# Kernel optimization log

Measured on AMD Instinct MI355X. Metric: run time of the kernel, lower is better.

Reference implementation:

```python
import jax, jax.numpy as jnp
import numpy as np

B, D, K = 4096, 1024, 32

def setup_inputs() -> dict:
    key = jax.random.key(0)
    k1, k2, k3, k4 = jax.random.split(key, 4)
    e1 = jax.random.normal(k1, (B, D), dtype=jnp.float32)
    e2 = jax.random.normal(k2, (B, D), dtype=jnp.float32)
    W = jax.random.normal(k3, (K, D, D), dtype=jnp.float32)
    V = jax.random.normal(k4, (2 * D, K), dtype=jnp.float32)
    b = jnp.zeros((D,), dtype=jnp.float32)
    return {"e1": e1, "e2": e2, "W": W, "V": V, "b": b}

def reference(e1, e2, W, V, b):
    batch = e1.shape[0]
    k = W.shape[0]
    # Per-slice bilinear form: btp[i, n] = sum_d e2[n,d] * (e1[n] @ W[i])[d] + sum(b)
    # (b is added elementwise before the axis-1 sum in the original, i.e. +sum(b))
    btp = jnp.einsum('bd,kde,be->kb', e1, W, e2) + jnp.sum(b)  # (k, B)
    # Original concatenates k (B,)-vectors along axis 0 then reshapes to (B, k);
    # reproduce that exact (interleaving) layout.
    btp = btp.reshape(batch, k)
    ff = jnp.concatenate([e1, e2], axis=-1) @ V  # (B, k)
    return jnp.tanh(btp + ff)
```

## Files before the change

kernel.cpp:

```cpp
#include <hip/hip_runtime.h>

#define B_SZ 4096
#define D_SZ 1024
#define K_SZ 32
#define NT   16

typedef _Float16 h16x8 __attribute__((ext_vector_type(8)));
typedef float f32x16 __attribute__((ext_vector_type(16)));
typedef float f32x4 __attribute__((ext_vector_type(4)));
typedef float f32x2 __attribute__((ext_vector_type(2)));
typedef unsigned int u32x2 __attribute__((ext_vector_type(2)));
typedef unsigned int u32x4 __attribute__((ext_vector_type(4)));
typedef unsigned short u16x4 __attribute__((ext_vector_type(4)));

#define GLOAD16(gp, sp) __builtin_amdgcn_global_load_lds( \
    (const __attribute__((address_space(1))) void*)(gp),  \
    (__attribute__((address_space(3))) void*)(sp), 16, 0, 0)

__device__ __forceinline__ void split1(float x, _Float16& h, _Float16& l) {
    h = (_Float16)x;
    l = (_Float16)((x - (float)h) * 2048.0f);
}

__global__ __launch_bounds__(256)
void ntl_prep_w(const float* __restrict__ W,
                _Float16* __restrict__ Wh, _Float16* __restrict__ Wl) {
    __shared__ float tile[64 * 69];
    const int bid = blockIdx.x;
    const int k  = bid >> 8;
    const int d0 = ((bid >> 4) & 15) << 6;
    const int e0 = (bid & 15) << 6;
    const int t  = threadIdx.x;
    const int r  = t >> 4;
    const int c4 = (t & 15) << 2;

    const float* src = W + ((size_t)k * D_SZ + d0) * D_SZ + e0;
    #pragma unroll
    for (int p = 0; p < 4; ++p) {
        f32x4 v = *(const f32x4*)(src + (size_t)(p * 16 + r) * D_SZ + c4);
        float* dst = &tile[(p * 16 + r) * 69 + c4];
        dst[0] = v[0]; dst[1] = v[1]; dst[2] = v[2]; dst[3] = v[3];
    }
    __syncthreads();
    #pragma unroll
    for (int p = 0; p < 4; ++p) {
        const int e = p * 16 + r;
        u16x4 hh, ll;
        #pragma unroll
        for (int q = 0; q < 4; ++q) {
            float v = tile[(c4 + q) * 69 + e];
            _Float16 h, l;
            split1(v, h, l);
            hh[q] = __builtin_bit_cast(unsigned short, h);
            ll[q] = __builtin_bit_cast(unsigned short, l);
        }
        const size_t o = ((size_t)k * D_SZ + e0 + e) * D_SZ + d0 + c4;
        *(u16x4*)(Wh + o) = hh;
        *(u16x4*)(Wl + o) = ll;
    }
}

__global__ __launch_bounds__(256)
void ntl_prep_e(const float* __restrict__ e1,
                _Float16* __restrict__ eh, _Float16* __restrict__ el) {
    const size_t i = ((size_t)blockIdx.x * 256 + threadIdx.x) * 4;
    f32x4 v = *(const f32x4*)(e1 + i);
    u16x4 hh, ll;
    #pragma unroll
    for (int q = 0; q < 4; ++q) {
        _Float16 h, l;
        split1(v[q], h, l);
        hh[q] = __builtin_bit_cast(unsigned short, h);
        ll[q] = __builtin_bit_cast(unsigned short, l);
    }
    *(u16x4*)(eh + i) = hh;
    *(u16x4*)(el + i) = ll;
}

__global__ __launch_bounds__(512, 2)
void ntl_bilinear4(const _Float16* __restrict__ eh, const _Float16* __restrict__ el,
                   const _Float16* __restrict__ Wh, const _Float16* __restrict__ Wl,
                   const float* __restrict__ e2, float* __restrict__ out) {
    __shared__ __align__(16) char lds[131072];

    const int bid   = blockIdx.x;
    const int xcd   = bid & 7;
    const int idx   = bid >> 3;
    const int e_t   = idx & 7;
    const int b_sub = (idx >> 3) & 1;
    const int k     = idx >> 4;
    const int b0    = (xcd * 2 + b_sub) * 256;
    const int e0    = e_t * 128;

    const int t    = threadIdx.x;
    const int l    = t & 63;
    const int w    = t >> 6;
    const int wrow = (w >> 1) * 64;
    const int wcol = (w & 1) * 64;
    const int l31  = l & 31;
    const int h5   = l >> 5;
    const int srow = l >> 3;
    const int sl   = l & 7;

    f32x16 acc1[2][2];
    f32x16 acc2[2][2];
    #pragma unroll
    for (int m = 0; m < 2; ++m)
        #pragma unroll
        for (int n = 0; n < 2; ++n) {
            #pragma unroll
            for (int j = 0; j < 16; ++j) { acc1[m][n][j] = 0.f; acc2[m][n][j] = 0.f; }
        }

    const size_t arow = (size_t)(b0 + w * 32 + srow) * D_SZ + sl * 8;
    const _Float16* gAh = eh + arow;
    const _Float16* gAl = el + arow;
    const int awOff = (w * 32 + srow) * 128 + ((sl ^ srow) << 4);

    const int gslot = sl ^ srow;
    const _Float16* gB = (w < 4 ? Wh : Wl) +
        ((size_t)k * D_SZ + e0 + (w & 3) * 32 + srow) * D_SZ + gslot * 8;
    const int bOff = (w >= 4 ? 16384 : 0) + (w & 3) * 4096;

    u32x4 arH[4], arL[4];

    {
        char* bset = lds + 65536;
        #pragma unroll
        for (int i = 0; i < 4; ++i)
            GLOAD16(gB + (size_t)i * 8 * D_SZ, bset + bOff + i * 1024);
        #pragma unroll
        for (int i = 0; i < 4; ++i) {
            arH[i] = *(const u32x4*)(gAh + (size_t)i * 8 * D_SZ);
            arL[i] = *(const u32x4*)(gAl + (size_t)i * 8 * D_SZ);
        }
    }

    for (int kt = 0; kt < NT; ++kt) {
        if (kt) {
            __builtin_amdgcn_s_barrier();
            __builtin_amdgcn_sched_barrier(0);
        }
        asm volatile("s_waitcnt vmcnt(0)" ::: "memory");
        __builtin_amdgcn_sched_barrier(0);

        #pragma unroll
        for (int i = 0; i < 4; ++i) {
            *(u32x4*)(lds + awOff + i * 1024)         = arH[i];
            *(u32x4*)(lds + 32768 + awOff + i * 1024) = arL[i];
        }

        if (kt + 1 < NT) {
            const size_t dn = (size_t)(kt + 1) * 64;
            char* bset = lds + 65536 + (((kt + 1) & 1) << 15);
            #pragma unroll
            for (int i = 0; i < 4; ++i)
                GLOAD16(gB + (size_t)i * 8 * D_SZ + dn, bset + bOff + i * 1024);
            #pragma unroll
            for (int i = 0; i < 4; ++i) {
                arH[i] = *(const u32x4*)(gAh + (size_t)i * 8 * D_SZ + dn);
                arL[i] = *(const u32x4*)(gAl + (size_t)i * 8 * D_SZ + dn);
            }
        }

        asm volatile("s_waitcnt lgkmcnt(0)" ::: "memory");
        __builtin_amdgcn_sched_barrier(0);
        __builtin_amdgcn_s_barrier();
        __builtin_amdgcn_sched_barrier(0);

        const char* Bh_ = lds + 65536 + ((kt & 1) << 15);
        const char* Bl_ = Bh_ + 16384;

        #pragma unroll
        for (int ks = 0; ks < 4; ++ks) {
            h16x8 ah[2], al[2], bh[2], bl[2];
            #pragma unroll
            for (int m = 0; m < 2; ++m) {
                const int r = wrow + m * 32 + l31;
                const int off = r * 128 + (((ks * 2 + h5) ^ (r & 7)) << 4);
                ah[m] = *(const h16x8*)(lds + off);
                al[m] = *(const h16x8*)(lds + 32768 + off);
            }
            #pragma unroll
            for (int n = 0; n < 2; ++n) {
                const int r = wcol + n * 32 + l31;
                const int off = r * 128 + (((ks * 2 + h5) ^ (r & 7)) << 4);
                bh[n] = *(const h16x8*)(Bh_ + off);
                bl[n] = *(const h16x8*)(Bl_ + off);
            }
            #pragma unroll
            for (int m = 0; m < 2; ++m)
                #pragma unroll
                for (int n = 0; n < 2; ++n) {
                    acc1[m][n] = __builtin_amdgcn_mfma_f32_32x32x16_f16(ah[m], bh[n], acc1[m][n], 0, 0, 0);
                    acc2[m][n] = __builtin_amdgcn_mfma_f32_32x32x16_f16(ah[m], bl[n], acc2[m][n], 0, 0, 0);
                    acc2[m][n] = __builtin_amdgcn_mfma_f32_32x32x16_f16(al[m], bh[n], acc2[m][n], 0, 0, 0);
                }
        }
    }

    float rsum[2][16];
    #pragma unroll
    for (int m = 0; m < 2; ++m)
        #pragma unroll
        for (int rg = 0; rg < 16; ++rg) rsum[m][rg] = 0.f;

    #pragma unroll
    for (int m = 0; m < 2; ++m) {
        #pragma unroll
        for (int n = 0; n < 2; ++n) {
            #pragma unroll
            for (int rg = 0; rg < 16; ++rg) {
                const int rowl = wrow + m * 32 + (rg & 3) + 8 * (rg >> 2) + 4 * h5;
                const int col  = e0 + wcol + n * 32 + l31;
                float tv = acc1[m][n][rg] + acc2[m][n][rg] * (1.0f / 2048.0f);
                rsum[m][rg] += tv * e2[(size_t)(b0 + rowl) * D_SZ + col];
            }
        }
    }

    #pragma unroll
    for (int m = 0; m < 2; ++m) {
        #pragma unroll
        for (int rg = 0; rg < 16; ++rg) {
            float v = rsum[m][rg];
            v += __shfl_xor(v, 1, 32);
            v += __shfl_xor(v, 2, 32);
            v += __shfl_xor(v, 4, 32);
            v += __shfl_xor(v, 8, 32);
            v += __shfl_xor(v, 16, 32);
            if (l31 == 0) {
                const int rowl = wrow + m * 32 + (rg & 3) + 8 * (rg >> 2) + 4 * h5;
                atomicAdd(out + (size_t)k * B_SZ + b0 + rowl, v);
            }
        }
    }
}

__device__ __forceinline__ int swz_fb(int row, int byte_in_row) {
    int slot = byte_in_row >> 4;
    int in   = byte_in_row & 15;
    return row * 128 + (((slot ^ (row & 7)) << 4) | in);
}
__device__ __forceinline__ void split_fb(float x, unsigned short& h, unsigned short& l) {
    _Float16 hf = (_Float16)x;
    float hff = (float)hf;
    _Float16 lf = (_Float16)((x - hff) * 2048.0f);
    h = __builtin_bit_cast(unsigned short, hf);
    l = __builtin_bit_cast(unsigned short, lf);
}
__global__ __launch_bounds__(256, 2)
void ntl_bilinear_fb(const float* __restrict__ e1, const float* __restrict__ e2,
                     const float* __restrict__ W, float* __restrict__ out) {
    __shared__ __align__(16) char smem[65536];
    char* const Ah = smem;
    char* const Al = smem + 16384;
    char* const Bh = smem + 32768;
    char* const Bl = smem + 49152;
    const int bid = blockIdx.x;
    const int k   = bid >> 8;
    const int rem = bid & 255;
    const int b0  = (rem >> 3) * 128;
    const int e0  = (rem & 7) * 128;
    const int t  = threadIdx.x;
    const int l  = t & 63;
    const int w  = t >> 6;
    const int wr = (w >> 1) * 64;
    const int wc = (w & 1) * 64;
    const int lrow = l & 15;
    const int lq   = l >> 4;
    f32x4 acc1[4][4], acc2[4][4];
    #pragma unroll
    for (int m = 0; m < 4; ++m)
        #pragma unroll
        for (int n = 0; n < 4; ++n) {
            acc1[m][n] = f32x4{0.f, 0.f, 0.f, 0.f};
            acc2[m][n] = f32x4{0.f, 0.f, 0.f, 0.f};
        }
    const int sa_row = t >> 4;
    const int sa_cg  = (t & 15) * 4;
    const int sb_e   = t & 127;
    const int sb_dg  = t >> 7;
    const float* const e1b = e1 + (size_t)b0 * D_SZ;
    const float* const wb  = W + ((size_t)k * D_SZ) * D_SZ + e0 + sb_e;
    for (int kt = 0; kt < NT; ++kt) {
        const int d0 = kt * 64;
        #pragma unroll
        for (int p = 0; p < 8; ++p) {
            const int r = sa_row + p * 16;
            f32x4 v = *(const f32x4*)(e1b + (size_t)r * D_SZ + d0 + sa_cg);
            unsigned short hh[4], ll[4];
            #pragma unroll
            for (int qq = 0; qq < 4; ++qq) split_fb(v[qq], hh[qq], ll[qq]);
            u32x2 hv = { (unsigned)hh[0] | ((unsigned)hh[1] << 16),
                         (unsigned)hh[2] | ((unsigned)hh[3] << 16) };
            u32x2 lv = { (unsigned)ll[0] | ((unsigned)ll[1] << 16),
                         (unsigned)ll[2] | ((unsigned)ll[3] << 16) };
            const int ad = swz_fb(r, sa_cg * 2);
            *(u32x2*)(Ah + ad) = hv;
            *(u32x2*)(Al + ad) = lv;
        }
        {
            const float* ws2 = wb + (size_t)(d0 + sb_dg * 32) * D_SZ;
            #pragma unroll
            for (int gg = 0; gg < 4; ++gg) {
                unsigned short hh[8], ll[8];
                #pragma unroll
                for (int i = 0; i < 8; ++i)
                    split_fb(ws2[(size_t)(gg * 8 + i) * D_SZ], hh[i], ll[i]);
                u32x4 hv = { (unsigned)hh[0] | ((unsigned)hh[1] << 16),
                             (unsigned)hh[2] | ((unsigned)hh[3] << 16),
                             (unsigned)hh[4] | ((unsigned)hh[5] << 16),
                             (unsigned)hh[6] | ((unsigned)hh[7] << 16) };
                u32x4 lv = { (unsigned)ll[0] | ((unsigned)ll[1] << 16),
                             (unsigned)ll[2] | ((unsigned)ll[3] << 16),
                             (unsigned)ll[4] | ((unsigned)ll[5] << 16),
                             (unsigned)ll[6] | ((unsigned)ll[7] << 16) };
                const int ad = swz_fb(sb_e, (sb_dg * 32 + gg * 8) * 2);
                *(u32x4*)(Bh + ad) = hv;
                *(u32x4*)(Bl + ad) = lv;
            }
        }
        __syncthreads();
        #pragma unroll
        for (int kk = 0; kk < 2; ++kk) {
            const int kb = kk * 64 + lq * 16;
            h16x8 a_h[4], a_l[4];
            #pragma unroll
            for (int m = 0; m < 4; ++m) {
                const int ad = swz_fb(wr + m * 16 + lrow, kb);
                a_h[m] = *(const h16x8*)(Ah + ad);
                a_l[m] = *(const h16x8*)(Al + ad);
            }
            #pragma unroll
            for (int n = 0; n < 4; ++n) {
                const int bd = swz_fb(wc + n * 16 + lrow, kb);
                h16x8 b_h = *(const h16x8*)(Bh + bd);
                h16x8 b_l = *(const h16x8*)(Bl + bd);
                #pragma unroll
                for (int m = 0; m < 4; ++m) {
                    acc1[m][n] = __builtin_amdgcn_mfma_f32_16x16x32_f16(a_h[m], b_h, acc1[m][n], 0, 0, 0);
                    acc2[m][n] = __builtin_amdgcn_mfma_f32_16x16x32_f16(a_h[m], b_l, acc2[m][n], 0, 0, 0);
                    acc2[m][n] = __builtin_amdgcn_mfma_f32_16x16x32_f16(a_l[m], b_h, acc2[m][n], 0, 0, 0);
                }
            }
        }
        __syncthreads();
    }
    float rsum[16];
    #pragma unroll
    for (int i = 0; i < 16; ++i) rsum[i] = 0.f;
    #pragma unroll
    for (int m = 0; m < 4; ++m) {
        #pragma unroll
        for (int n = 0; n < 4; ++n) {
            const int col = e0 + wc + n * 16 + lrow;
            #pragma unroll
            for (int j = 0; j < 4; ++j) {
                const int row = b0 + wr + m * 16 + lq * 4 + j;
                float tv = acc1[m][n][j] + acc2[m][n][j] * (1.0f / 2048.0f);
                rsum[m * 4 + j] += tv * e2[(size_t)row * D_SZ + col];
            }
        }
    }
    #pragma unroll
    for (int i = 0; i < 16; ++i) {
        float v = rsum[i];
        v += __shfl_xor(v, 1, 16);
        v += __shfl_xor(v, 2, 16);
        v += __shfl_xor(v, 4, 16);
        v += __shfl_xor(v, 8, 16);
        if (lrow == 0) {
            const int row = b0 + wr + (i >> 2) * 16 + lq * 4 + (i & 3);
            atomicAdd(out + (size_t)k * B_SZ + row, v);
        }
    }
}

__global__ __launch_bounds__(256)
void ntl_ff(const float* __restrict__ e1, const float* __restrict__ e2,
            const float* __restrict__ V, float* __restrict__ out) {
    __shared__ float vt[32 * 258];
    const int t  = threadIdx.x;
    const int c  = t & 31;
    const int rl = t >> 5;
    const int r  = blockIdx.x * 8 + rl;
    float acc = 0.f;
    for (int j0 = 0; j0 < 2 * D_SZ; j0 += 256) {
        __syncthreads();
        #pragma unroll
        for (int i = 0; i < 32; ++i) {
            const int f = i * 256 + t;
            vt[(f & 31) * 258 + (f >> 5)] = V[(size_t)j0 * K_SZ + f];
        }
        __syncthreads();
        const float* src = (j0 < D_SZ) ? (e1 + (size_t)r * D_SZ + j0)
                                       : (e2 + (size_t)r * D_SZ + (j0 - D_SZ));
        #pragma unroll 8
        for (int jj = 0; jj < 256; jj += 2) {
            f32x2 a  = *(const f32x2*)(src + jj);
            f32x2 vv = *(const f32x2*)(&vt[c * 258 + jj]);
            acc += a[0] * vv[0] + a[1] * vv[1];
        }
    }
    out[(size_t)r * K_SZ + c] += acc;
}

__global__ void ntl_sumb(const float* __restrict__ b, float* __restrict__ ws) {
    __shared__ float red[256];
    const int t = threadIdx.x;
    red[t] = b[t] + b[t + 256] + b[t + 512] + b[t + 768];
    __syncthreads();
    for (int s = 128; s > 0; s >>= 1) {
        if (t < s) red[t] += red[t + s];
        __syncthreads();
    }
    if (t == 0) ws[0] = red[0];
}

__global__ void ntl_tanh(float* __restrict__ out, const float* __restrict__ ws) {
    const int p = blockIdx.x * 256 + threadIdx.x;
    out[p] = tanhf(out[p] + ws[0]);
}

extern "C" void kernel_launch(void* const* d_in, const int* in_sizes, int n_in,
                              void* d_out, int out_size, void* d_ws, size_t ws_size,
                              hipStream_t stream) {
    const float* e1 = (const float*)d_in[0];
    const float* e2 = (const float*)d_in[1];
    const float* W  = (const float*)d_in[2];
    const float* V  = (const float*)d_in[3];
    const float* b  = (const float*)d_in[4];
    float* out = (float*)d_out;

    const size_t WT = (size_t)K_SZ * D_SZ * D_SZ;
    const size_t ET = (size_t)B_SZ * D_SZ;
    const size_t need = (2 * WT + 2 * ET) * sizeof(_Float16) + 16;

    hipMemsetAsync(d_out, 0, (size_t)B_SZ * K_SZ * sizeof(float), stream);

    if (ws_size >= need) {
        _Float16* Wh = (_Float16*)d_ws;
        _Float16* Wl = Wh + WT;
        _Float16* eh = Wl + WT;
        _Float16* el = eh + ET;
        float* sb = (float*)(el + ET);
        ntl_sumb<<<1, 256, 0, stream>>>(b, sb);
        ntl_prep_w<<<dim3(K_SZ * 256), dim3(256), 0, stream>>>(W, Wh, Wl);
        ntl_prep_e<<<dim3((int)(ET / 1024)), dim3(256), 0, stream>>>(e1, eh, el);
        ntl_bilinear4<<<dim3(4096), dim3(512), 0, stream>>>(eh, el, Wh, Wl, e2, out);
        ntl_ff<<<dim3(B_SZ / 8), dim3(256), 0, stream>>>(e1, e2, V, out);
        ntl_tanh<<<dim3((B_SZ * K_SZ) / 256), dim3(256), 0, stream>>>(out, sb);
    } else {
        float* sb = (float*)d_ws;
        ntl_sumb<<<1, 256, 0, stream>>>(b, sb);
        ntl_bilinear_fb<<<dim3(K_SZ * 256), dim3(256), 0, stream>>>(e1, e2, W, out);
        ntl_ff<<<dim3(B_SZ / 8), dim3(256), 0, stream>>>(e1, e2, V, out);
        ntl_tanh<<<dim3((B_SZ * K_SZ) / 256), dim3(256), 0, stream>>>(out, sb);
    }
}
```

Measured before the change: 947.0 us.

## Stage A and B tiles via direct global-to-LDS loads with smaller K step

The bilinear MFMA kernel now loads both the e1 split halves and the W split halves straight into LDS with global_load_lds, instead of staging A through registers and ds_write. The K tile shrinks from 64 to 32, so there are twice as many iterations, and LDS use drops to 96KB with a new two-row-per-line swizzle and precomputed read offsets. The epilogue swaps 32 separate shuffle reductions and 32 atomics per lane group for a transposed butterfly reduction, so each lane issues a single atomicAdd. The cost is more barriers per output tile, since each iteration ends in a full __syncthreads.

```diff
diff --git a/kernel.cpp b/kernel.cpp
--- a/kernel.cpp
+++ b/kernel.cpp
@@ -3,7 +3,7 @@
 #define B_SZ 4096
 #define D_SZ 1024
 #define K_SZ 32
-#define NT   16
+#define NT   32
 
 typedef _Float16 h16x8 __attribute__((ext_vector_type(8)));
 typedef float f32x16 __attribute__((ext_vector_type(16)));
@@ -78,10 +78,10 @@
 }
 
 __global__ __launch_bounds__(512, 2)
-void ntl_bilinear4(const _Float16* __restrict__ eh, const _Float16* __restrict__ el,
+void ntl_bilinear5(const _Float16* __restrict__ eh, const _Float16* __restrict__ el,
                    const _Float16* __restrict__ Wh, const _Float16* __restrict__ Wl,
                    const float* __restrict__ e2, float* __restrict__ out) {
-    __shared__ __align__(16) char lds[131072];
+    __shared__ __align__(16) char lds[98304];
 
     const int bid   = blockIdx.x;
     const int xcd   = bid & 7;
@@ -99,8 +99,6 @@
     const int wcol = (w & 1) * 64;
     const int l31  = l & 31;
     const int h5   = l >> 5;
-    const int srow = l >> 3;
-    const int sl   = l & 7;
 
     f32x16 acc1[2][2];
     f32x16 acc2[2][2];
@@ -112,81 +110,70 @@
             for (int j = 0; j < 16; ++j) { acc1[m][n][j] = 0.f; acc2[m][n][j] = 0.f; }
         }
 
-    const size_t arow = (size_t)(b0 + w * 32 + srow) * D_SZ + sl * 8;
-    const _Float16* gAh = eh + arow;
-    const _Float16* gAl = el + arow;
-    const int awOff = (w * 32 + srow) * 128 + ((sl ^ srow) << 4);
-
-    const int gslot = sl ^ srow;
-    const _Float16* gB = (w < 4 ? Wh : Wl) +
-        ((size_t)k * D_SZ + e0 + (w & 3) * 32 + srow) * D_SZ + gslot * 8;
-    const int bOff = (w >= 4 ? 16384 : 0) + (w & 3) * 4096;
-
-    u32x4 arH[4], arL[4];
-
-    {
-        char* bset = lds + 65536;
-        #pragma unroll
-        for (int i = 0; i < 4; ++i)
-            GLOAD16(gB + (size_t)i * 8 * D_SZ, bset + bOff + i * 1024);
-        #pragma unroll
-        for (int i = 0; i < 4; ++i) {
-            arH[i] = *(const u32x4*)(gAh + (size_t)i * 8 * D_SZ);
-            arL[i] = *(const u32x4*)(gAl + (size_t)i * 8 * D_SZ);
-        }
-    }
+    const int slx  = (l & 7) ^ (l >> 3);
+    const int lrow = 2 * (l >> 3) + (slx >> 2);
+    const int kg   = slx & 3;
+
+    const _Float16* gA0h = eh + (size_t)(b0 + 32 * w + lrow) * D_SZ + kg * 8;
+    const _Float16* gA1h = gA0h + (size_t)16 * D_SZ;
+    const _Float16* gA0l = el + (size_t)(b0 + 32 * w + lrow) * D_SZ + kg * 8;
+    const _Float16* gA1l = gA0l + (size_t)16 * D_SZ;
+    const _Float16* gBh  = Wh + ((size_t)k * D_SZ + e0 + 16 * w + lrow) * D_SZ + kg * 8;
+    const _Float16* gBl  = Wl + ((size_t)k * D_SZ + e0 + 16 * w + lrow) * D_SZ + kg * 8;
+
+    int aoff[2][2], boff[2][2];
+    #pragma unroll
+    for (int m = 0; m < 2; ++m) {
+        const int r = wrow + m * 32 + l31;
+        const int line = r >> 1;
+        const int pr = (r & 1) << 2;
+        #pragma unroll
+        for (int ks = 0; ks < 2; ++ks)
+            aoff[m][ks] = line * 128 + (((pr | (ks * 2 + h5)) ^ (line & 7)) << 4);
+    }
+    #pragma unroll
+    for (int n = 0; n < 2; ++n) {
+        const int r = wcol + n * 32 + l31;
+        const int line = r >> 1;
+        const int pr = (r & 1) << 2;
+        #pragma unroll
+        for (int ks = 0; ks < 2; ++ks)
+            boff[n][ks] = line * 128 + (((pr | (ks * 2 + h5)) ^ (line & 7)) << 4);
+    }
+
+#define STAGE(bufbase, ktv) do {                                   \
+        const size_t kb = (size_t)(ktv) * 32;                      \
+        char* bb = (bufbase);                                      \
+        GLOAD16(gA0h + kb, bb + w * 2048);                         \
+        GLOAD16(gA1h + kb, bb + w * 2048 + 1024);                  \
+        GLOAD16(gA0l + kb, bb + 16384 + w * 2048);                 \
+        GLOAD16(gA1l + kb, bb + 16384 + w * 2048 + 1024);          \
+        GLOAD16(gBh + kb,  bb + 32768 + w * 1024);                 \
+        GLOAD16(gBl + kb,  bb + 40960 + w * 1024);                 \
+    } while (0)
+
+    STAGE(lds, 0);
+    __syncthreads();
 
     for (int kt = 0; kt < NT; ++kt) {
-        if (kt) {
-            __builtin_amdgcn_s_barrier();
+        if (kt + 1 < NT) {
+            STAGE(lds + (((kt + 1) & 1) ? 49152 : 0), kt + 1);
             __builtin_amdgcn_sched_barrier(0);
         }
-        asm volatile("s_waitcnt vmcnt(0)" ::: "memory");
-        __builtin_amdgcn_sched_barrier(0);
-
-        #pragma unroll
-        for (int i = 0; i < 4; ++i) {
-            *(u32x4*)(lds + awOff + i * 1024)         = arH[i];
-            *(u32x4*)(lds + 32768 + awOff + i * 1024) = arL[i];
-        }
-
-        if (kt + 1 < NT) {
-            const size_t dn = (size_t)(kt + 1) * 64;
-            char* bset = lds + 65536 + (((kt + 1) & 1) << 15);
-            #pragma unroll
-            for (int i = 0; i < 4; ++i)
-                GLOAD16(gB + (size_t)i * 8 * D_SZ + dn, bset + bOff + i * 1024);
-            #pragma unroll
-            for (int i = 0; i < 4; ++i) {
-                arH[i] = *(const u32x4*)(gAh + (size_t)i * 8 * D_SZ + dn);
-                arL[i] = *(const u32x4*)(gAl + (size_t)i * 8 * D_SZ + dn);
-            }
-        }
-
-        asm volatile("s_waitcnt lgkmcnt(0)" ::: "memory");
-        __builtin_amdgcn_sched_barrier(0);
-        __builtin_amdgcn_s_barrier();
-        __builtin_amdgcn_sched_barrier(0);
-
-        const char* Bh_ = lds + 65536 + ((kt & 1) << 15);
-        const char* Bl_ = Bh_ + 16384;
-
-        #pragma unroll
-        for (int ks = 0; ks < 4; ++ks) {
+
+        const char* bufc = lds + ((kt & 1) ? 49152 : 0);
+        #pragma unroll
+        for (int ks = 0; ks < 2; ++ks) {
             h16x8 ah[2], al[2], bh[2], bl[2];
             #pragma unroll
             for (int m = 0; m < 2; ++m) {
-                const int r = wrow + m * 32 + l31;
-                const int off = r * 128 + (((ks * 2 + h5) ^ (r & 7)) << 4);
-                ah[m] = *(const h16x8*)(lds + off);
-                al[m] = *(const h16x8*)(lds + 32768 + off);
+                ah[m] = *(const h16x8*)(bufc + aoff[m][ks]);
+                al[m] = *(const h16x8*)(bufc + 16384 + aoff[m][ks]);
             }
             #pragma unroll
             for (int n = 0; n < 2; ++n) {
-                const int r = wcol + n * 32 + l31;
-                const int off = r * 128 + (((ks * 2 + h5) ^ (r & 7)) << 4);
-                bh[n] = *(const h16x8*)(Bh_ + off);
-                bl[n] = *(const h16x8*)(Bl_ + off);
+                bh[n] = *(const h16x8*)(bufc + 32768 + boff[n][ks]);
+                bl[n] = *(const h16x8*)(bufc + 40960 + boff[n][ks]);
             }
             #pragma unroll
             for (int m = 0; m < 2; ++m)
@@ -197,44 +184,43 @@
                     acc2[m][n] = __builtin_amdgcn_mfma_f32_32x32x16_f16(al[m], bh[n], acc2[m][n], 0, 0, 0);
                 }
         }
-    }
-
-    float rsum[2][16];
-    #pragma unroll
-    for (int m = 0; m < 2; ++m)
-        #pragma unroll
-        for (int rg = 0; rg < 16; ++rg) rsum[m][rg] = 0.f;
+        __syncthreads();
+    }
+#undef STAGE
+
+    float v[32];
+    #pragma unroll
+    for (int j = 0; j < 32; ++j) v[j] = 0.f;
 
     #pragma unroll
     for (int m = 0; m < 2; ++m) {
         #pragma unroll
         for (int n = 0; n < 2; ++n) {
+            const int col = e0 + wcol + n * 32 + l31;
             #pragma unroll
             for (int rg = 0; rg < 16; ++rg) {
-                const int rowl = wrow + m * 32 + (rg & 3) + 8 * (rg >> 2) + 4 * h5;
-                const int col  = e0 + wcol + n * 32 + l31;
+                const int row = b0 + wrow + m * 32 + (rg & 3) + 8 * (rg >> 2) + 4 * h5;
                 float tv = acc1[m][n][rg] + acc2[m][n][rg] * (1.0f / 2048.0f);
-                rsum[m][rg] += tv * e2[(size_t)(b0 + rowl) * D_SZ + col];
-            }
-        }
-    }
-
-    #pragma unroll
-    for (int m = 0; m < 2; ++m) {
-        #pragma unroll
-        for (int rg = 0; rg < 16; ++rg) {
-            float v = rsum[m][rg];
-            v += __shfl_xor(v, 1, 32);
-            v += __shfl_xor(v, 2, 32);
-            v += __shfl_xor(v, 4, 32);
-            v += __shfl_xor(v, 8, 32);
-            v += __shfl_xor(v, 16, 32);
-            if (l31 == 0) {
-                const int rowl = wrow + m * 32 + (rg & 3) + 8 * (rg >> 2) + 4 * h5;
-                atomicAdd(out + (size_t)k * B_SZ + b0 + rowl, v);
-            }
-        }
-    }
+                v[m * 16 + rg] += tv * e2[(size_t)row * D_SZ + col];
+            }
+        }
+    }
+
+    #pragma unroll
+    for (int s = 0; s < 5; ++s) {
+        const int half = 16 >> s;
+        const bool hi = (l31 >> s) & 1;
+        #pragma unroll
+        for (int i = 0; i < half; ++i) {
+            float send = hi ? v[i] : v[i + half];
+            float recv = __shfl_xor(send, 1 << s, 32);
+            v[i] = (hi ? v[i + half] : v[i]) + recv;
+        }
+    }
+
+    const int j = ((l31 & 1) << 4) | ((l31 & 2) << 2) | (l31 & 4) | ((l31 & 8) >> 2) | ((l31 & 16) >> 4);
+    const int row = wrow + (j >> 4) * 32 + (j & 3) + 8 * ((j >> 2) & 3) + 4 * h5;
+    atomicAdd(out + (size_t)k * B_SZ + b0 + row, v[0]);
 }
 
 __device__ __forceinline__ int swz_fb(int row, int byte_in_row) {
@@ -283,15 +269,15 @@
     const int sb_dg  = t >> 7;
     const float* const e1b = e1 + (size_t)b0 * D_SZ;
     const float* const wb  = W + ((size_t)k * D_SZ) * D_SZ + e0 + sb_e;
-    for (int kt = 0; kt < NT; ++kt) {
+    for (int kt = 0; kt < 16; ++kt) {
         const int d0 = kt * 64;
         #pragma unroll
         for (int p = 0; p < 8; ++p) {
             const int r = sa_row + p * 16;
-            f32x4 v = *(const f32x4*)(e1b + (size_t)r * D_SZ + d0 + sa_cg);
+            f32x4 vv4 = *(const f32x4*)(e1b + (size_t)r * D_SZ + d0 + sa_cg);
             unsigned short hh[4], ll[4];
             #pragma unroll
-            for (int qq = 0; qq < 4; ++qq) split_fb(v[qq], hh[qq], ll[qq]);
+            for (int qq = 0; qq < 4; ++qq) split_fb(vv4[qq], hh[qq], ll[qq]);
             u32x2 hv = { (unsigned)hh[0] | ((unsigned)hh[1] << 16),
                          (unsigned)hh[2] | ((unsigned)hh[3] << 16) };
             u32x2 lv = { (unsigned)ll[0] | ((unsigned)ll[1] << 16),
@@ -356,23 +342,23 @@
         for (int n = 0; n < 4; ++n) {
             const int col = e0 + wc + n * 16 + lrow;
             #pragma unroll
-            for (int j = 0; j < 4; ++j) {
-                const int row = b0 + wr + m * 16 + lq * 4 + j;
-                float tv = acc1[m][n][j] + acc2[m][n][j] * (1.0f / 2048.0f);
-                rsum[m * 4 + j] += tv * e2[(size_t)row * D_SZ + col];
+            for (int jq = 0; jq < 4; ++jq) {
+                const int row = b0 + wr + m * 16 + lq * 4 + jq;
+                float tv = acc1[m][n][jq] + acc2[m][n][jq] * (1.0f / 2048.0f);
+                rsum[m * 4 + jq] += tv * e2[(size_t)row * D_SZ + col];
             }
         }
     }
     #pragma unroll
     for (int i = 0; i < 16; ++i) {
-        float v = rsum[i];
-        v += __shfl_xor(v, 1, 16);
-        v += __shfl_xor(v, 2, 16);
-        v += __shfl_xor(v, 4, 16);
-        v += __shfl_xor(v, 8, 16);
+        float vv = rsum[i];
+        vv += __shfl_xor(vv, 1, 16);
+        vv += __shfl_xor(vv, 2, 16);
+        vv += __shfl_xor(vv, 4, 16);
+        vv += __shfl_xor(vv, 8, 16);
         if (lrow == 0) {
             const int row = b0 + wr + (i >> 2) * 16 + lq * 4 + (i & 3);
-            atomicAdd(out + (size_t)k * B_SZ + row, v);
+            atomicAdd(out + (size_t)k * B_SZ + row, vv);
         }
     }
 }
@@ -442,13 +428,13 @@
     if (ws_size >= need) {
         _Float16* Wh = (_Float16*)d_ws;
         _Float16* Wl = Wh + WT;
-        _Float16* eh = Wl + WT;
-        _Float16* el = eh + ET;
-        float* sb = (float*)(el + ET);
+        _Float16* ehp = Wl + WT;
+        _Float16* elp = ehp + ET;
+        float* sb = (float*)(elp + ET);
         ntl_sumb<<<1, 256, 0, stream>>>(b, sb);
         ntl_prep_w<<<dim3(K_SZ * 256), dim3(256), 0, stream>>>(W, Wh, Wl);
-        ntl_prep_e<<<dim3((int)(ET / 1024)), dim3(256), 0, stream>>>(e1, eh, el);
-        ntl_bilinear4<<<dim3(4096), dim3(512), 0, stream>>>(eh, el, Wh, Wl, e2, out);
+        ntl_prep_e<<<dim3((int)(ET / 1024)), dim3(256), 0, stream>>>(e1, ehp, elp);
+        ntl_bilinear5<<<dim3(4096), dim3(512), 0, stream>>>(ehp, elp, Wh, Wl, e2, out);
         ntl_ff<<<dim3(B_SZ / 8), dim3(256), 0, stream>>>(e1, e2, V, out);
         ntl_tanh<<<dim3((B_SZ * K_SZ) / 256), dim3(256), 0, stream>>>(out, sb);
     } else {
```

Result: slower. 1.115 ms (+17.7%).
